# Performance work log

Measured on AMD Instinct MI355X. Metric: run time of the kernel, lower is better.

Reference implementation:

```python
import jax, jax.numpy as jnp
import numpy as np

N, E, M, D = 100000, 50000, 1000000, 128  # vertices, hyperedges, incidences, hidden


def setup_inputs() -> dict:
    key = jax.random.key(0)
    ks = jax.random.split(key, 9)
    v = jax.random.normal(ks[0], (N, D), dtype=jnp.float32)
    e = jax.random.normal(ks[1], (E, D), dtype=jnp.float32)
    vidx = jax.random.randint(ks[2], (M,), 0, N)
    eidx = jax.random.randint(ks[3], (M,), 0, E)
    v_reg_weight = jax.random.uniform(ks[4], (M, 1), dtype=jnp.float32)
    e_reg_weight = jax.random.uniform(ks[5], (M, 1), dtype=jnp.float32)
    v_reg_sum = jnp.ones((N, 1), dtype=jnp.float32)
    e_reg_sum = jnp.ones((E, 1), dtype=jnp.float32)
    # learned parameters
    W_v2e = jax.random.normal(ks[6], (D, D), dtype=jnp.float32)
    W_e2v = jax.random.normal(ks[7], (D, D), dtype=jnp.float32)
    b_v = jnp.zeros((D,), dtype=jnp.float32)
    b_e = jnp.zeros((D,), dtype=jnp.float32)
    v_weight = jax.random.uniform(ks[8], (N, 1), dtype=jnp.float32)  # args.v_weight
    return dict(v=v, e=e, vidx=vidx, eidx=eidx,
                v_reg_weight=v_reg_weight, e_reg_weight=e_reg_weight,
                v_reg_sum=v_reg_sum, e_reg_sum=e_reg_sum,
                W_v2e=W_v2e, W_e2v=W_e2v, b_v=b_v, b_e=b_e, v_weight=v_weight)


def reference(v, e, vidx, eidx, v_reg_weight, e_reg_weight, v_reg_sum, e_reg_sum,
              W_v2e, W_e2v, b_v, b_e, v_weight):
    # v2e: dense transform, gather by vidx, reweight, scatter_add into edges
    ve = jax.nn.relu(v @ W_v2e + b_v)                      # [N, D]
    v_out = v * v_weight * 4.0                             # v_fac = 4
    msg_ve = (ve * v_weight)[vidx] * v_reg_weight          # [M, D]
    e_out = e + jax.ops.segment_sum(msg_ve, eidx, num_segments=E)
    e_out = e_out / e_reg_sum
    # e2v: dense transform, gather by eidx, reweight, scatter_add into vertices
    ev = jax.nn.relu(e_out @ W_e2v + b_e)                  # [E, D]
    msg_ev = (ev / 3.0)[eidx] * e_reg_weight               # [M, D]
    v_out = v_out + jax.ops.segment_sum(msg_ev, vidx, num_segments=N)
    v_out = v_out / v_reg_sum
    # is_last_mod=True: no dropout
    return v_out, e_out
```

## Files before the change

kernel.cpp:

```cpp
#include <hip/hip_runtime.h>
#include <cstddef>

#define DD 128
#define PART_ELEMS 4096
#define MAXB 256
#define MAXW 512
#define WT_LD 136

typedef __attribute__((ext_vector_type(8))) short bf16x8;
typedef __attribute__((ext_vector_type(4))) float f32x4;

__device__ __forceinline__ unsigned bf16pk(float x, float y) {
    unsigned a = __float_as_uint(x);
    unsigned b = __float_as_uint(y);
    a = (a + 0x7FFFu + ((a >> 16) & 1u)) >> 16;
    b = (b + 0x7FFFu + ((b >> 16) & 1u)) >> 16;
    return a | (b << 16);
}
__device__ __forceinline__ unsigned short bf16r(float x) {
    unsigned u = __float_as_uint(x);
    return (unsigned short)((u + 0x7FFFu + ((u >> 16) & 1u)) >> 16);
}
__device__ __forceinline__ float bflo(unsigned u) { return __uint_as_float(u << 16); }
__device__ __forceinline__ float bfhi(unsigned u) { return __uint_as_float(u & 0xFFFF0000u); }

__global__ __launch_bounds__(256)
void conv_w_kernel(const float* __restrict__ W0, const float* __restrict__ W1,
                   unsigned short* __restrict__ Wt0, unsigned short* __restrict__ Wt1,
                   int* __restrict__ bcur_e, int* __restrict__ bcur_v, int e_cap, int v_cap)
{
    int idx = blockIdx.x * 256 + threadIdx.x;
    int k = idx >> 7, c = idx & 127;
    Wt0[c * 128 + k] = bf16r(W0[idx]);
    Wt1[c * 128 + k] = bf16r(W1[idx]);
    if (blockIdx.x == 0) {
        bcur_e[threadIdx.x] = threadIdx.x * e_cap;
        bcur_v[threadIdx.x] = threadIdx.x * v_cap;
    }
}

__global__ __launch_bounds__(256)
void part2_kernel(const int* __restrict__ eidx, const int* __restrict__ vidx,
                  const float* __restrict__ vrw, const float* __restrict__ erw,
                  int* __restrict__ bcur_e, int* __restrict__ bcur_v,
                  int2* __restrict__ tmp_e, int2* __restrict__ tmp_v,
                  int M, int e_shift, int v_shift, int e_bk, int v_bk)
{
    __shared__ int lcnt_e[MAXB], lbase_e[MAXB], lcnt_v[MAXB], lbase_v[MAXB];
    const int t = threadIdx.x;
    const int base = blockIdx.x * PART_ELEMS;
    const int end = min(base + PART_ELEMS, M);

    if (t < e_bk) lcnt_e[t] = 0;
    if (t < v_bk) lcnt_v[t] = 0;
    __syncthreads();
    for (int j = base + t; j < end; j += 256) {
        atomicAdd(&lcnt_e[eidx[j] >> e_shift], 1);
        atomicAdd(&lcnt_v[vidx[j] >> v_shift], 1);
    }
    __syncthreads();
    if (t < e_bk) { int c = lcnt_e[t]; lbase_e[t] = c ? atomicAdd(&bcur_e[t], c) : 0; lcnt_e[t] = 0; }
    if (t < v_bk) { int c = lcnt_v[t]; lbase_v[t] = c ? atomicAdd(&bcur_v[t], c) : 0; lcnt_v[t] = 0; }
    __syncthreads();
    for (int j = base + t; j < end; j += 256) {
        int ei = eidx[j], vi = vidx[j];
        int wqe = (int)(vrw[j] * 32767.0f + 0.5f); wqe = wqe < 32767 ? wqe : 32767;
        int wqv = (int)(erw[j] * 32767.0f + 0.5f); wqv = wqv < 32767 ? wqv : 32767;
        int be = ei >> e_shift;
        int pe = lbase_e[be] + atomicAdd(&lcnt_e[be], 1);
        tmp_e[pe] = make_int2(ei | (wqe << 17), vi);
        int bv = vi >> v_shift;
        int pv = lbase_v[bv] + atomicAdd(&lcnt_v[bv], 1);
        tmp_v[pv] = make_int2(vi | (wqv << 17), ei);
    }
}

struct FineLds { int lcnt[MAXW]; int lstart[MAXW]; int sdata[256]; int scnt[256]; int spbase; };
struct GemmLds { unsigned short Wt[128 * WT_LD]; unsigned short At[64 * WT_LD]; };

__device__ __forceinline__
void fine_body(int blk, FineLds& L,
               const int2* __restrict__ tmp_e, const int* __restrict__ bcur_e,
               int e_cap, int e_shift, int En, int e_bk,
               int* __restrict__ e_start, unsigned* __restrict__ e_pack,
               const int2* __restrict__ tmp_v, const int* __restrict__ bcur_v,
               int v_cap, int v_shift, int Nn, int v_bk,
               int* __restrict__ v_start, unsigned* __restrict__ v_pack, int M)
{
    const int t = threadIdx.x;
    const int2* tmp; const int* bcur; int cap, shift, n, nb, b;
    int* start; unsigned* pack;
    if (blk < e_bk) {
        tmp = tmp_e; bcur = bcur_e; cap = e_cap; shift = e_shift; n = En; nb = e_bk;
        start = e_start; pack = e_pack; b = blk;
    } else {
        tmp = tmp_v; bcur = bcur_v; cap = v_cap; shift = v_shift; n = Nn; nb = v_bk;
        start = v_start; pack = v_pack; b = blk - e_bk;
    }

    int cnt_t = (t < nb) ? (bcur[t] - t * cap) : 0;
    L.scnt[t] = cnt_t;
    __syncthreads();
    int xx = cnt_t;
    for (int off = 1; off < 256; off <<= 1) {
        int y = (t >= off) ? L.scnt[t - off] : 0;
        __syncthreads();
        xx += y;
        L.scnt[t] = xx;
        __syncthreads();
    }
    if (t == b) L.spbase = xx - cnt_t;
    if (b == nb - 1 && t == 0) start[n] = M;
    __syncthreads();
    const int pbase = L.spbase;

    const int d0 = b << shift;
    const int width = min(1 << shift, n - d0);
    const int tbase = b * cap;
    const int nrec = bcur[b] - tbase;

    L.lcnt[t] = 0; L.lcnt[t + 256] = 0;
    __syncthreads();
    for (int j = t; j < nrec; j += 256)
        atomicAdd(&L.lcnt[(tmp[tbase + j].x & 0x1FFFF) - d0], 1);
    __syncthreads();
    int a = L.lcnt[2 * t], bb = L.lcnt[2 * t + 1];
    int s = a + bb;
    L.sdata[t] = s;
    __syncthreads();
    int x = s;
    for (int off = 1; off < 256; off <<= 1) {
        int y = (t >= off) ? L.sdata[t - off] : 0;
        __syncthreads();
        x += y;
        L.sdata[t] = x;
        __syncthreads();
    }
    int ex = x - s;
    L.lstart[2 * t] = ex;
    L.lstart[2 * t + 1] = ex + a;
    L.lcnt[2 * t] = 0; L.lcnt[2 * t + 1] = 0;
    __syncthreads();
    for (int i = t; i < width; i += 256)
        start[d0 + i] = pbase + L.lstart[i];
    for (int j = t; j < nrec; j += 256) {
        int2 r = tmp[tbase + j];
        int di = (r.x & 0x1FFFF) - d0;
        int pos = pbase + L.lstart[di] + atomicAdd(&L.lcnt[di], 1);
        pack[pos] = (unsigned)r.y | (((unsigned)r.x >> 17) << 17);
    }
}

__device__ __forceinline__
void gemm_body(int blk, GemmLds& L, const float* __restrict__ A,
               const unsigned short* __restrict__ Wtg, const float* __restrict__ bias,
               const float* __restrict__ rowwt, unsigned* __restrict__ outb,
               int nrows, float scale, bool v2e)
{
    const int t = threadIdx.x;
    const int row0 = blk * 64;

    {
        int r = t >> 1, h = t & 1;
        const uint4* src = reinterpret_cast<const uint4*>(Wtg + r * 128 + h * 64);
        uint4* dst = reinterpret_cast<uint4*>(&L.Wt[r * WT_LD + h * 64]);
        #pragma unroll
        for (int i = 0; i < 8; ++i) dst[i] = src[i];
    }
    {
        int r = t >> 2, q = t & 3;
        int grow = row0 + r;
        uint4 o[4];
        if (grow < nrows) {
            const float4* src = reinterpret_cast<const float4*>(A + (size_t)grow * DD + q * 32);
            #pragma unroll
            for (int i = 0; i < 4; ++i) {
                float4 f0 = src[2 * i];
                float4 f1 = src[2 * i + 1];
                o[i].x = bf16pk(f0.x, f0.y);
                o[i].y = bf16pk(f0.z, f0.w);
                o[i].z = bf16pk(f1.x, f1.y);
                o[i].w = bf16pk(f1.z, f1.w);
            }
        } else {
            #pragma unroll
            for (int i = 0; i < 4; ++i) o[i] = make_uint4(0, 0, 0, 0);
        }
        uint4* dst = reinterpret_cast<uint4*>(&L.At[r * WT_LD + q * 32]);
        #pragma unroll
        for (int i = 0; i < 4; ++i) dst[i] = o[i];
    }
    __syncthreads();

    const int w  = t >> 6;
    const int l  = t & 63;
    const int lr = l & 15;
    const int lk = (l >> 4) * 8;

    f32x4 acc[8];
    #pragma unroll
    for (int i = 0; i < 8; ++i) acc[i] = 0.0f;

    const int arow = w * 16 + lr;
    #pragma unroll
    for (int ks = 0; ks < 4; ++ks) {
        bf16x8 af = *reinterpret_cast<const bf16x8*>(&L.At[arow * WT_LD + lk + ks * 32]);
        #pragma unroll
        for (int ct = 0; ct < 8; ++ct) {
            bf16x8 bfr = *reinterpret_cast<const bf16x8*>(&L.Wt[(ct * 16 + lr) * WT_LD + lk + ks * 32]);
            acc[ct] = __builtin_amdgcn_mfma_f32_16x16x32_bf16(af, bfr, acc[ct], 0, 0, 0);
        }
    }

    float bcol[8];
    #pragma unroll
    for (int ct = 0; ct < 8; ++ct) bcol[ct] = bias[ct * 16 + lr];
    #pragma unroll
    for (int r = 0; r < 4; ++r) {
        int rl = w * 16 + (l >> 4) * 4 + r;
        int grow = row0 + rl;
        float rw = scale;
        if (v2e) rw = (grow < nrows) ? rowwt[grow] : 0.f;
        #pragma unroll
        for (int ct = 0; ct < 8; ++ct) {
            float val = fmaxf(acc[ct][r] + bcol[ct], 0.f) * rw;
            L.At[rl * WT_LD + ct * 16 + lr] = bf16r(val);
        }
    }
    {
        int r = t >> 2, part = t & 3;
        int grow = row0 + r;
        if (grow < nrows) {
            const uint4* src = reinterpret_cast<const uint4*>(&L.At[r * WT_LD + part * 32]);
            uint4* dst = reinterpret_cast<uint4*>(outb + (size_t)grow * 64 + part * 16);
            dst[0] = src[0]; dst[1] = src[1]; dst[2] = src[2]; dst[3] = src[3];
        }
    }
}

__global__ __launch_bounds__(256)
void fused_fine_gemm_kernel(const int2* __restrict__ tmp_e, const int* __restrict__ bcur_e,
                            int e_cap, int e_shift, int En, int e_bk,
                            int* __restrict__ e_start, unsigned* __restrict__ e_pack,
                            const int2* __restrict__ tmp_v, const int* __restrict__ bcur_v,
                            int v_cap, int v_shift, int Nn, int v_bk,
                            int* __restrict__ v_start, unsigned* __restrict__ v_pack, int M,
                            const float* __restrict__ v, const unsigned short* __restrict__ Wt0,
                            const float* __restrict__ bv, const float* __restrict__ vweight,
                            unsigned* __restrict__ vwb)
{
    __shared__ union SM { FineLds f; GemmLds g; } sm;
    const int nfine = e_bk + v_bk;
    if ((int)blockIdx.x < nfine) {
        fine_body(blockIdx.x, sm.f, tmp_e, bcur_e, e_cap, e_shift, En, e_bk, e_start, e_pack,
                  tmp_v, bcur_v, v_cap, v_shift, Nn, v_bk, v_start, v_pack, M);
    } else {
        gemm_body(blockIdx.x - nfine, sm.g, v, Wt0, bv, vweight, vwb, Nn, 1.0f, true);
    }
}

__global__ __launch_bounds__(256)
void gemm_mfma_kernel(const float* __restrict__ A, const unsigned short* __restrict__ Wtg,
                      const float* __restrict__ bias, unsigned* __restrict__ outb,
                      int nrows, float scale)
{
    __shared__ GemmLds sm;
    gemm_body(blockIdx.x, sm, A, Wtg, bias, nullptr, outb, nrows, scale, false);
}

__global__ __launch_bounds__(256)
void e_agg_kernel(const float* __restrict__ e, const unsigned* __restrict__ vwb,
                  const int* __restrict__ start, const unsigned* __restrict__ pack,
                  const float* __restrict__ ers, float* __restrict__ eout, int E)
{
    int row = blockIdx.x * 4 + (threadIdx.x >> 6);
    if (row >= E) return;
    int lane = threadIdx.x & 63;
    int qw = lane >> 4;
    int ql = lane & 15;
    int s = start[row], t = start[row + 1];

    float a0=0.f,a1=0.f,a2=0.f,a3=0.f,a4=0.f,a5=0.f,a6=0.f,a7=0.f;
    float b0=0.f,b1=0.f,b2=0.f,b3=0.f,b4=0.f,b5=0.f,b6=0.f,b7=0.f;

    int j = s;
    for (; j + 8 <= t; j += 8) {
        unsigned pw0 = pack[j + qw];
        unsigned pw1 = pack[j + 4 + qw];
        uint4 u0 = *reinterpret_cast<const uint4*>(&vwb[(size_t)(pw0 & 0x1FFFFu) * 64 + ql * 4]);
        uint4 u1 = *reinterpret_cast<const uint4*>(&vwb[(size_t)(pw1 & 0x1FFFFu) * 64 + ql * 4]);
        float w0 = (float)(pw0 >> 17) * (1.0f / 32767.0f);
        float w1 = (float)(pw1 >> 17) * (1.0f / 32767.0f);
        a0 = fmaf(bflo(u0.x), w0, a0); a1 = fmaf(bfhi(u0.x), w0, a1);
        a2 = fmaf(bflo(u0.y), w0, a2); a3 = fmaf(bfhi(u0.y), w0, a3);
        a4 = fmaf(bflo(u0.z), w0, a4); a5 = fmaf(bfhi(u0.z), w0, a5);
        a6 = fmaf(bflo(u0.w), w0, a6); a7 = fmaf(bfhi(u0.w), w0, a7);
        b0 = fmaf(bflo(u1.x), w1, b0); b1 = fmaf(bfhi(u1.x), w1, b1);
        b2 = fmaf(bflo(u1.y), w1, b2); b3 = fmaf(bfhi(u1.y), w1, b3);
        b4 = fmaf(bflo(u1.z), w1, b4); b5 = fmaf(bfhi(u1.z), w1, b5);
        b6 = fmaf(bflo(u1.w), w1, b6); b7 = fmaf(bfhi(u1.w), w1, b7);
    }
    for (; j < t; j += 4) {
        int jj = j + qw;
        if (jj < t) {
            unsigned pw = pack[jj];
            float wm = (float)(pw >> 17) * (1.0f / 32767.0f);
            uint4 u = *reinterpret_cast<const uint4*>(&vwb[(size_t)(pw & 0x1FFFFu) * 64 + ql * 4]);
            a0 = fmaf(bflo(u.x), wm, a0); a1 = fmaf(bfhi(u.x), wm, a1);
            a2 = fmaf(bflo(u.y), wm, a2); a3 = fmaf(bfhi(u.y), wm, a3);
            a4 = fmaf(bflo(u.z), wm, a4); a5 = fmaf(bfhi(u.z), wm, a5);
            a6 = fmaf(bflo(u.w), wm, a6); a7 = fmaf(bfhi(u.w), wm, a7);
        }
    }
    float r0 = a0 + b0, r1 = a1 + b1, r2 = a2 + b2, r3 = a3 + b3;
    float r4 = a4 + b4, r5 = a5 + b5, r6 = a6 + b6, r7 = a7 + b7;
    r0 += __shfl_xor(r0, 16, 64); r0 += __shfl_xor(r0, 32, 64);
    r1 += __shfl_xor(r1, 16, 64); r1 += __shfl_xor(r1, 32, 64);
    r2 += __shfl_xor(r2, 16, 64); r2 += __shfl_xor(r2, 32, 64);
    r3 += __shfl_xor(r3, 16, 64); r3 += __shfl_xor(r3, 32, 64);
    r4 += __shfl_xor(r4, 16, 64); r4 += __shfl_xor(r4, 32, 64);
    r5 += __shfl_xor(r5, 16, 64); r5 += __shfl_xor(r5, 32, 64);
    r6 += __shfl_xor(r6, 16, 64); r6 += __shfl_xor(r6, 32, 64);
    r7 += __shfl_xor(r7, 16, 64); r7 += __shfl_xor(r7, 32, 64);
    if (qw == 0) {
        float rs = 1.0f / ers[row];
        const float4* ep = reinterpret_cast<const float4*>(&e[(size_t)row * DD + ql * 8]);
        float4 e0 = ep[0], e1 = ep[1];
        float4 o0 = make_float4((e0.x + r0) * rs, (e0.y + r1) * rs, (e0.z + r2) * rs, (e0.w + r3) * rs);
        float4 o1 = make_float4((e1.x + r4) * rs, (e1.y + r5) * rs, (e1.z + r6) * rs, (e1.w + r7) * rs);
        float4* op = reinterpret_cast<float4*>(&eout[(size_t)row * DD + ql * 8]);
        op[0] = o0; op[1] = o1;
    }
}

__global__ __launch_bounds__(256)
void v_agg_kernel(const float* __restrict__ v, const unsigned* __restrict__ evb,
                  const int* __restrict__ start, const unsigned* __restrict__ pack,
                  const float* __restrict__ vrs, const float* __restrict__ vweight,
                  float* __restrict__ vout, int N)
{
    int row = blockIdx.x * 4 + (threadIdx.x >> 6);
    if (row >= N) return;
    int lane = threadIdx.x & 63;
    int qw = lane >> 4;
    int ql = lane & 15;
    int s = start[row], t = start[row + 1];

    float a0=0.f,a1=0.f,a2=0.f,a3=0.f,a4=0.f,a5=0.f,a6=0.f,a7=0.f;
    float b0=0.f,b1=0.f,b2=0.f,b3=0.f,b4=0.f,b5=0.f,b6=0.f,b7=0.f;

    int j = s;
    for (; j + 8 <= t; j += 8) {
        unsigned pw0 = pack[j + qw];
        unsigned pw1 = pack[j + 4 + qw];
        uint4 u0 = *reinterpret_cast<const uint4*>(&evb[(size_t)(pw0 & 0x1FFFFu) * 64 + ql * 4]);
        uint4 u1 = *reinterpret_cast<const uint4*>(&evb[(size_t)(pw1 & 0x1FFFFu) * 64 + ql * 4]);
        float w0 = (float)(pw0 >> 17) * (1.0f / 32767.0f);
        float w1 = (float)(pw1 >> 17) * (1.0f / 32767.0f);
        a0 = fmaf(bflo(u0.x), w0, a0); a1 = fmaf(bfhi(u0.x), w0, a1);
        a2 = fmaf(bflo(u0.y), w0, a2); a3 = fmaf(bfhi(u0.y), w0, a3);
        a4 = fmaf(bflo(u0.z), w0, a4); a5 = fmaf(bfhi(u0.z), w0, a5);
        a6 = fmaf(bflo(u0.w), w0, a6); a7 = fmaf(bfhi(u0.w), w0, a7);
        b0 = fmaf(bflo(u1.x), w1, b0); b1 = fmaf(bfhi(u1.x), w1, b1);
        b2 = fmaf(bflo(u1.y), w1, b2); b3 = fmaf(bfhi(u1.y), w1, b3);
        b4 = fmaf(bflo(u1.z), w1, b4); b5 = fmaf(bfhi(u1.z), w1, b5);
        b6 = fmaf(bflo(u1.w), w1, b6); b7 = fmaf(bfhi(u1.w), w1, b7);
    }
    for (; j < t; j += 4) {
        int jj = j + qw;
        if (jj < t) {
            unsigned pw = pack[jj];
            float wm = (float)(pw >> 17) * (1.0f / 32767.0f);
            uint4 u = *reinterpret_cast<const uint4*>(&evb[(size_t)(pw & 0x1FFFFu) * 64 + ql * 4]);
            a0 = fmaf(bflo(u.x), wm, a0); a1 = fmaf(bfhi(u.x), wm, a1);
            a2 = fmaf(bflo(u.y), wm, a2); a3 = fmaf(bfhi(u.y), wm, a3);
            a4 = fmaf(bflo(u.z), wm, a4); a5 = fmaf(bfhi(u.z), wm, a5);
            a6 = fmaf(bflo(u.w), wm, a6); a7 = fmaf(bfhi(u.w), wm, a7);
        }
    }
    float r0 = a0 + b0, r1 = a1 + b1, r2 = a2 + b2, r3 = a3 + b3;
    float r4 = a4 + b4, r5 = a5 + b5, r6 = a6 + b6, r7 = a7 + b7;
    r0 += __shfl_xor(r0, 16, 64); r0 += __shfl_xor(r0, 32, 64);
    r1 += __shfl_xor(r1, 16, 64); r1 += __shfl_xor(r1, 32, 64);
    r2 += __shfl_xor(r2, 16, 64); r2 += __shfl_xor(r2, 32, 64);
    r3 += __shfl_xor(r3, 16, 64); r3 += __shfl_xor(r3, 32, 64);
    r4 += __shfl_xor(r4, 16, 64); r4 += __shfl_xor(r4, 32, 64);
    r5 += __shfl_xor(r5, 16, 64); r5 += __shfl_xor(r5, 32, 64);
    r6 += __shfl_xor(r6, 16, 64); r6 += __shfl_xor(r6, 32, 64);
    r7 += __shfl_xor(r7, 16, 64); r7 += __shfl_xor(r7, 32, 64);
    if (qw == 0) {
        float rs = 1.0f / vrs[row];
        float wt = vweight[row] * 4.0f;
        const float4* vp = reinterpret_cast<const float4*>(&v[(size_t)row * DD + ql * 8]);
        float4 v0 = vp[0], v1 = vp[1];
        float4 o0 = make_float4((v0.x * wt + r0) * rs, (v0.y * wt + r1) * rs,
                                (v0.z * wt + r2) * rs, (v0.w * wt + r3) * rs);
        float4 o1 = make_float4((v1.x * wt + r4) * rs, (v1.y * wt + r5) * rs,
                                (v1.z * wt + r6) * rs, (v1.w * wt + r7) * rs);
        float4* op = reinterpret_cast<float4*>(&vout[(size_t)row * DD + ql * 8]);
        op[0] = o0; op[1] = o1;
    }
}

extern "C" void kernel_launch(void* const* d_in, const int* in_sizes, int n_in,
                              void* d_out, int out_size, void* d_ws, size_t ws_size,
                              hipStream_t stream)
{
    const float* v       = (const float*)d_in[0];
    const float* e       = (const float*)d_in[1];
    const int*   vidx    = (const int*)d_in[2];
    const int*   eidx    = (const int*)d_in[3];
    const float* vrw     = (const float*)d_in[4];
    const float* erw     = (const float*)d_in[5];
    const float* vrs     = (const float*)d_in[6];
    const float* ers     = (const float*)d_in[7];
    const float* Wv2e    = (const float*)d_in[8];
    const float* We2v    = (const float*)d_in[9];
    const float* bv      = (const float*)d_in[10];
    const float* be      = (const float*)d_in[11];
    const float* vweight = (const float*)d_in[12];

    const int N = in_sizes[0] / DD;
    const int E = in_sizes[1] / DD;
    const int M = in_sizes[2];

    float* vout = (float*)d_out;
    float* eout = vout + (size_t)N * DD;

    auto calc_shift = [](int n) {
        int s = 0;
        while (((n + (1 << s) - 1) >> s) > MAXB) ++s;
        return s;
    };
    const int e_shift = calc_shift(E);
    const int v_shift = calc_shift(N);
    const int e_bk = (E + (1 << e_shift) - 1) >> e_shift;
    const int v_bk = (N + (1 << v_shift) - 1) >> v_shift;
    const int e_cap = ((M / e_bk) * 3) / 2 + 256;
    const int v_cap = ((M / v_bk) * 3) / 2 + 256;

    char* wsb = (char*)d_ws;
    size_t off = 0;
    auto alloc = [&](size_t bytes) { char* p = wsb + off; off += (bytes + 255) & ~(size_t)255; return p; };
    unsigned* vwb   = (unsigned*)alloc((size_t)N * 64 * sizeof(unsigned));
    unsigned* evb   = vwb;
    int*   e_start = (int*)alloc((size_t)(E + 1) * sizeof(int));
    int*   v_start = (int*)alloc((size_t)(N + 1) * sizeof(int));
    int*   bcur_e  = (int*)alloc(MAXB * sizeof(int));
    int*   bcur_v  = (int*)alloc(MAXB * sizeof(int));
    unsigned short* Wt0 = (unsigned short*)alloc(DD * DD * sizeof(unsigned short));
    unsigned short* Wt1 = (unsigned short*)alloc(DD * DD * sizeof(unsigned short));
    unsigned* e_pack = (unsigned*)alloc((size_t)M * sizeof(unsigned));
    unsigned* v_pack = (unsigned*)alloc((size_t)M * sizeof(unsigned));
    int2*  tmp_e   = (int2*)alloc((size_t)e_bk * e_cap * sizeof(int2));
    int2*  tmp_v   = (int2*)alloc((size_t)v_bk * v_cap * sizeof(int2));

    const int pblk = (M + PART_ELEMS - 1) / PART_ELEMS;
    const int gblkN = (N + 63) / 64;

    conv_w_kernel<<<64, 256, 0, stream>>>(Wv2e, We2v, Wt0, Wt1, bcur_e, bcur_v, e_cap, v_cap);
    part2_kernel<<<pblk, 256, 0, stream>>>(eidx, vidx, vrw, erw, bcur_e, bcur_v,
                                           tmp_e, tmp_v, M, e_shift, v_shift, e_bk, v_bk);
    fused_fine_gemm_kernel<<<e_bk + v_bk + gblkN, 256, 0, stream>>>(
        tmp_e, bcur_e, e_cap, e_shift, E, e_bk, e_start, e_pack,
        tmp_v, bcur_v, v_cap, v_shift, N, v_bk, v_start, v_pack, M,
        v, Wt0, bv, vweight, vwb);
    e_agg_kernel<<<(E + 3) / 4, 256, 0, stream>>>(e, vwb, e_start, e_pack, ers, eout, E);
    gemm_mfma_kernel<<<(E + 63) / 64, 256, 0, stream>>>(eout, Wt1, be, evb, E, 1.0f / 3.0f);
    v_agg_kernel<<<(N + 3) / 4, 256, 0, stream>>>(v, evb, v_start, v_pack, vrs, vweight, vout, N);
}
```

Baseline: 181.7 us.

## Read GEMM weight fragments from global memory instead of staging them in LDS

```diff
diff --git a/kernel.cpp b/kernel.cpp
--- a/kernel.cpp
+++ b/kernel.cpp
@@ -26,17 +26,12 @@
 
 __global__ __launch_bounds__(256)
 void conv_w_kernel(const float* __restrict__ W0, const float* __restrict__ W1,
-                   unsigned short* __restrict__ Wt0, unsigned short* __restrict__ Wt1,
-                   int* __restrict__ bcur_e, int* __restrict__ bcur_v, int e_cap, int v_cap)
+                   unsigned short* __restrict__ Wt0, unsigned short* __restrict__ Wt1)
 {
     int idx = blockIdx.x * 256 + threadIdx.x;
     int k = idx >> 7, c = idx & 127;
     Wt0[c * 128 + k] = bf16r(W0[idx]);
     Wt1[c * 128 + k] = bf16r(W1[idx]);
-    if (blockIdx.x == 0) {
-        bcur_e[threadIdx.x] = threadIdx.x * e_cap;
-        bcur_v[threadIdx.x] = threadIdx.x * v_cap;
-    }
 }
 
 __global__ __launch_bounds__(256)
@@ -44,7 +39,8 @@
                   const float* __restrict__ vrw, const float* __restrict__ erw,
                   int* __restrict__ bcur_e, int* __restrict__ bcur_v,
                   int2* __restrict__ tmp_e, int2* __restrict__ tmp_v,
-                  int M, int e_shift, int v_shift, int e_bk, int v_bk)
+                  int M, int e_shift, int v_shift, int e_bk, int v_bk,
+                  int e_cap, int v_cap)
 {
     __shared__ int lcnt_e[MAXB], lbase_e[MAXB], lcnt_v[MAXB], lbase_v[MAXB];
     const int t = threadIdx.x;
@@ -59,8 +55,8 @@
         atomicAdd(&lcnt_v[vidx[j] >> v_shift], 1);
     }
     __syncthreads();
-    if (t < e_bk) { int c = lcnt_e[t]; lbase_e[t] = c ? atomicAdd(&bcur_e[t], c) : 0; lcnt_e[t] = 0; }
-    if (t < v_bk) { int c = lcnt_v[t]; lbase_v[t] = c ? atomicAdd(&bcur_v[t], c) : 0; lcnt_v[t] = 0; }
+    if (t < e_bk) { int c = lcnt_e[t]; lbase_e[t] = t * e_cap + (c ? atomicAdd(&bcur_e[t], c) : 0); lcnt_e[t] = 0; }
+    if (t < v_bk) { int c = lcnt_v[t]; lbase_v[t] = t * v_cap + (c ? atomicAdd(&bcur_v[t], c) : 0); lcnt_v[t] = 0; }
     __syncthreads();
     for (int j = base + t; j < end; j += 256) {
         int ei = eidx[j], vi = vidx[j];
@@ -76,7 +72,7 @@
 }
 
 struct FineLds { int lcnt[MAXW]; int lstart[MAXW]; int sdata[256]; int scnt[256]; int spbase; };
-struct GemmLds { unsigned short Wt[128 * WT_LD]; unsigned short At[64 * WT_LD]; };
+struct GemmLds { unsigned short At[64 * WT_LD]; };
 
 __device__ __forceinline__
 void fine_body(int blk, FineLds& L,
@@ -98,7 +94,7 @@
         start = v_start; pack = v_pack; b = blk - e_bk;
     }
 
-    int cnt_t = (t < nb) ? (bcur[t] - t * cap) : 0;
+    int cnt_t = (t < nb) ? bcur[t] : 0;
     L.scnt[t] = cnt_t;
     __syncthreads();
     int xx = cnt_t;
@@ -117,7 +113,7 @@
     const int d0 = b << shift;
     const int width = min(1 << shift, n - d0);
     const int tbase = b * cap;
-    const int nrec = bcur[b] - tbase;
+    const int nrec = bcur[b];
 
     L.lcnt[t] = 0; L.lcnt[t + 256] = 0;
     __syncthreads();
@@ -151,22 +147,16 @@
     }
 }
 
+template<bool V2E>
 __device__ __forceinline__
 void gemm_body(int blk, GemmLds& L, const float* __restrict__ A,
                const unsigned short* __restrict__ Wtg, const float* __restrict__ bias,
                const float* __restrict__ rowwt, unsigned* __restrict__ outb,
-               int nrows, float scale, bool v2e)
+               int nrows, float scale)
 {
     const int t = threadIdx.x;
     const int row0 = blk * 64;
 
-    {
-        int r = t >> 1, h = t & 1;
-        const uint4* src = reinterpret_cast<const uint4*>(Wtg + r * 128 + h * 64);
-        uint4* dst = reinterpret_cast<uint4*>(&L.Wt[r * WT_LD + h * 64]);
-        #pragma unroll
-        for (int i = 0; i < 8; ++i) dst[i] = src[i];
-    }
     {
         int r = t >> 2, q = t & 3;
         int grow = row0 + r;
@@ -207,7 +197,7 @@
         bf16x8 af = *reinterpret_cast<const bf16x8*>(&L.At[arow * WT_LD + lk + ks * 32]);
         #pragma unroll
         for (int ct = 0; ct < 8; ++ct) {
-            bf16x8 bfr = *reinterpret_cast<const bf16x8*>(&L.Wt[(ct * 16 + lr) * WT_LD + lk + ks * 32]);
+            bf16x8 bfr = *reinterpret_cast<const bf16x8*>(&Wtg[(ct * 16 + lr) * 128 + lk + ks * 32]);
             acc[ct] = __builtin_amdgcn_mfma_f32_16x16x32_bf16(af, bfr, acc[ct], 0, 0, 0);
         }
     }
@@ -220,7 +210,7 @@
         int rl = w * 16 + (l >> 4) * 4 + r;
         int grow = row0 + rl;
         float rw = scale;
-        if (v2e) rw = (grow < nrows) ? rowwt[grow] : 0.f;
+        if (V2E) rw = (grow < nrows) ? rowwt[grow] : 0.f;
         #pragma unroll
         for (int ct = 0; ct < 8; ++ct) {
             float val = fmaxf(acc[ct][r] + bcol[ct], 0.f) * rw;
@@ -255,7 +245,7 @@
         fine_body(blockIdx.x, sm.f, tmp_e, bcur_e, e_cap, e_shift, En, e_bk, e_start, e_pack,
                   tmp_v, bcur_v, v_cap, v_shift, Nn, v_bk, v_start, v_pack, M);
     } else {
-        gemm_body(blockIdx.x - nfine, sm.g, v, Wt0, bv, vweight, vwb, Nn, 1.0f, true);
+        gemm_body<true>(blockIdx.x - nfine, sm.g, v, Wt0, bv, vweight, vwb, Nn, 1.0f);
     }
 }
 
@@ -265,7 +255,7 @@
                       int nrows, float scale)
 {
     __shared__ GemmLds sm;
-    gemm_body(blockIdx.x, sm, A, Wtg, bias, nullptr, outb, nrows, scale, false);
+    gemm_body<false>(blockIdx.x, sm, A, Wtg, bias, nullptr, outb, nrows, scale);
 }
 
 __global__ __launch_bounds__(256)
@@ -458,9 +448,12 @@
     const int pblk = (M + PART_ELEMS - 1) / PART_ELEMS;
     const int gblkN = (N + 63) / 64;
 
-    conv_w_kernel<<<64, 256, 0, stream>>>(Wv2e, We2v, Wt0, Wt1, bcur_e, bcur_v, e_cap, v_cap);
+    hipMemsetAsync(bcur_e, 0, MAXB * sizeof(int), stream);
+    hipMemsetAsync(bcur_v, 0, MAXB * sizeof(int), stream);
+    conv_w_kernel<<<64, 256, 0, stream>>>(Wv2e, We2v, Wt0, Wt1);
     part2_kernel<<<pblk, 256, 0, stream>>>(eidx, vidx, vrw, erw, bcur_e, bcur_v,
-                                           tmp_e, tmp_v, M, e_shift, v_shift, e_bk, v_bk);
+                                           tmp_e, tmp_v, M, e_shift, v_shift, e_bk, v_bk,
+                                           e_cap, v_cap);
     fused_fine_gemm_kernel<<<e_bk + v_bk + gblkN, 256, 0, stream>>>(
         tmp_e, bcur_e, e_cap, e_shift, E, e_bk, e_start, e_pack,
         tmp_v, bcur_v, v_cap, v_shift, N, v_bk, v_start, v_pack, M,
```

Measured after the change: 205.3 us. +13.0%, slower.
